# Performance work log

Measured on AMD Instinct MI355X. Metric: run time of the kernel, lower is better.

## Reference

```python
import jax, jax.numpy as jnp
import numpy as np

NUM_HOPS = 8
SIGMA = 0.1
EPS = 1e-12  # torch F.normalize default eps


def _l2_normalize(x):
    # torch.nn.functional.normalize(x, dim=1): x / max(||x||_2, eps)
    norm = jnp.linalg.norm(x, axis=1, keepdims=True)
    return x / jnp.maximum(norm, EPS)


def setup_inputs() -> dict:
    key = jax.random.key(0)
    k1, k2 = jax.random.split(key)
    N, E, D = 100000, 3200000, 128
    x = jax.random.normal(k1, (N, D), dtype=jnp.float32)
    edge_index = jax.random.randint(k2, (2, E), 0, N, dtype=jnp.int64)
    return {"x": x, "edge_index": edge_index}


def reference(x, edge_index):
    # A[i, j] = 1 for each edge (i=src, j=dst); A^T @ h scatters h[src] into rows dst.
    # Duplicate edges coalesce by summation, matching torch sparse mm.
    N = x.shape[0]
    src = edge_index[0]
    dst = edge_index[1]
    noise_key = jax.random.key(42)
    cur = _l2_normalize(x)
    outs = [cur]
    for k in range(NUM_HOPS):
        aggr = jax.ops.segment_sum(cur[src], dst, num_segments=N)  # [N, D]
        noise = SIGMA * jax.random.normal(jax.random.fold_in(noise_key, k), aggr.shape, dtype=aggr.dtype)
        cur = _l2_normalize(aggr + noise)
        outs.append(cur)
    return jnp.stack(outs)  # [num_hops+1, N, D]
```

## Files before the change

### kernel.cpp

```cpp
#include <hip/hip_runtime.h>
#include <hip/hip_bf16.h>
#include <hip/hip_fp16.h>
#include <stdint.h>

#define D 128
#define NUM_HOPS 8
#define SCAN_BS 256
#define SCAN2_BS 512
#define FILLA_EPT 16

__host__ __device__ inline void tf2x32(uint32_t k0, uint32_t k1,
                                       uint32_t x0, uint32_t x1,
                                       uint32_t* o0, uint32_t* o1) {
  uint32_t ks2 = k0 ^ k1 ^ 0x1BD11BDAu;
  x0 += k0; x1 += k1;
#define TF_RND(r) { x0 += x1; x1 = (x1 << r) | (x1 >> (32 - r)); x1 ^= x0; }
  TF_RND(13) TF_RND(15) TF_RND(26) TF_RND(6)
  x0 += k1; x1 += ks2 + 1u;
  TF_RND(17) TF_RND(29) TF_RND(16) TF_RND(24)
  x0 += ks2; x1 += k0 + 2u;
  TF_RND(13) TF_RND(15) TF_RND(26) TF_RND(6)
  x0 += k0; x1 += k1 + 3u;
  TF_RND(17) TF_RND(29) TF_RND(16) TF_RND(24)
  x0 += k1; x1 += ks2 + 4u;
  TF_RND(13) TF_RND(15) TF_RND(26) TF_RND(6)
  x0 += ks2; x1 += k0 + 5u;
#undef TF_RND
  *o0 = x0; *o1 = x1;
}

__device__ inline float erfinv_f32(float x) {
  float w = -log1pf(-x * x);
  float p;
  if (w < 5.0f) {
    w = w - 2.5f;
    p = 2.81022636e-08f;
    p = fmaf(p, w, 3.43273939e-07f);
    p = fmaf(p, w, -3.5233877e-06f);
    p = fmaf(p, w, -4.39150654e-06f);
    p = fmaf(p, w, 0.00021858087f);
    p = fmaf(p, w, -0.00125372503f);
    p = fmaf(p, w, -0.00417768164f);
    p = fmaf(p, w, 0.246640727f);
    p = fmaf(p, w, 1.50140941f);
  } else {
    w = sqrtf(w) - 3.0f;
    p = -0.000200214257f;
    p = fmaf(p, w, 0.000100950558f);
    p = fmaf(p, w, 0.00134934322f);
    p = fmaf(p, w, -0.00367342844f);
    p = fmaf(p, w, 0.00573950773f);
    p = fmaf(p, w, -0.0076224613f);
    p = fmaf(p, w, 0.00943887047f);
    p = fmaf(p, w, 1.00167406f);
    p = fmaf(p, w, 2.83297682f);
  }
  return p * x;
}

__device__ inline float noise_from_bits(uint32_t bits) {
  const float lo = -0.99999994f;
  uint32_t fb = (bits >> 9) | 0x3f800000u;
  float f = __uint_as_float(fb) - 1.0f;
  float u = fmaxf(lo, fmaf(f, 2.0f, lo));
  return 0.1f * (1.41421354f * erfinv_f32(u));
}

__device__ inline float noise_elem(uint32_t fk0, uint32_t fk1, long t) {
  uint32_t o0, o1;
  tf2x32(fk0, fk1, (uint32_t)(((unsigned long)t) >> 32), (uint32_t)t, &o0, &o1);
  return noise_from_bits(o0 ^ o1);
}

__device__ inline bool edges_are_i64(const int* __restrict__ ei) {
  return (ei[1] | ei[3] | ei[5] | ei[7] | ei[9] | ei[11] | ei[13] | ei[15]) == 0;
}

__global__ __launch_bounds__(256) void hist_kernel(const int* __restrict__ ei,
                                                   int* __restrict__ counts, long E) {
  long e = (long)blockIdx.x * blockDim.x + threadIdx.x;
  if (e >= E) return;
  bool i64 = edges_are_i64(ei);
  int d = __builtin_nontemporal_load(&ei[i64 ? (2 * (E + e)) : (E + e)]);
  atomicAdd(&counts[d], 1);
}

__global__ __launch_bounds__(SCAN_BS) void scan1_kernel(const int* __restrict__ counts,
                                                        int* __restrict__ excl,
                                                        int* __restrict__ partials, int N) {
  __shared__ int lds[SCAN_BS];
  int tid = threadIdx.x;
  int i = blockIdx.x * SCAN_BS + tid;
  int v = (i < N) ? counts[i] : 0;
  lds[tid] = v;
  __syncthreads();
  for (int off = 1; off < SCAN_BS; off <<= 1) {
    int t = (tid >= off) ? lds[tid - off] : 0;
    __syncthreads();
    if (tid >= off) lds[tid] += t;
    __syncthreads();
  }
  int incl = lds[tid];
  if (i < N) excl[i] = incl - v;
  if (tid == SCAN_BS - 1) partials[blockIdx.x] = incl;
}

__global__ __launch_bounds__(SCAN2_BS) void scan2_kernel(int* __restrict__ partials, int nchunks) {
  __shared__ int lds[SCAN2_BS];
  int tid = threadIdx.x;
  int v = (tid < nchunks) ? partials[tid] : 0;
  lds[tid] = v;
  __syncthreads();
  for (int off = 1; off < SCAN2_BS; off <<= 1) {
    int t = (tid >= off) ? lds[tid - off] : 0;
    __syncthreads();
    if (tid >= off) lds[tid] += t;
    __syncthreads();
  }
  if (tid < nchunks) partials[tid] = lds[tid] - v;
}

__global__ __launch_bounds__(256) void scan3_kernel(int* __restrict__ row_ptr,
                                                    const int* __restrict__ partials,
                                                    int* __restrict__ cursor, int N, int E) {
  int i = blockIdx.x * blockDim.x + threadIdx.x;
  if (i > N) return;
  if (i == N) { row_ptr[N] = E; return; }
  int v = row_ptr[i] + partials[i >> 8];
  row_ptr[i] = v;
  cursor[i] = v;
}

__global__ __launch_bounds__(256) void bucket_init_kernel(const int* __restrict__ row_ptr,
                                                          int* __restrict__ bucketCursor,
                                                          int nb, int shift, int N) {
  int b = blockIdx.x * blockDim.x + threadIdx.x;
  if (b >= nb) return;
  long r = (long)b << shift;
  if (r > N) r = N;
  bucketCursor[b] = row_ptr[r];
}

__global__ __launch_bounds__(256) void fillA_kernel(const int* __restrict__ ei,
                                                    int* __restrict__ bucketCursor,
                                                    uint64_t* __restrict__ tmp,
                                                    long E, int shift, int nb) {
  __shared__ int ldsCount[256];
  __shared__ int ldsBase[256];
  __shared__ int ldsRank[256];
  int tid = threadIdx.x;
  long base = (long)blockIdx.x * (256 * FILLA_EPT);
  bool i64 = edges_are_i64(ei);

  int  sv[FILLA_EPT], dv[FILLA_EPT];
  ldsCount[tid] = 0; ldsRank[tid] = 0;
  __syncthreads();

  #pragma unroll
  for (int j = 0; j < FILLA_EPT; ++j) {
    long e = base + tid + (long)j * 256;
    if (e < E) {
      sv[j] = __builtin_nontemporal_load(&ei[i64 ? (2 * e) : e]);
      dv[j] = __builtin_nontemporal_load(&ei[i64 ? (2 * (E + e)) : (E + e)]);
      atomicAdd(&ldsCount[dv[j] >> shift], 1);
    } else { sv[j] = -1; dv[j] = -1; }
  }
  __syncthreads();
  if (tid < nb && ldsCount[tid] > 0)
    ldsBase[tid] = atomicAdd(&bucketCursor[tid], ldsCount[tid]);
  __syncthreads();
  #pragma unroll
  for (int j = 0; j < FILLA_EPT; ++j) {
    if (dv[j] >= 0) {
      int b = dv[j] >> shift;
      int r = atomicAdd(&ldsRank[b], 1);
      tmp[ldsBase[b] + r] = ((uint64_t)(uint32_t)dv[j] << 32) | (uint32_t)sv[j];
    }
  }
}

__global__ __launch_bounds__(256) void fillB_kernel(const uint64_t* __restrict__ tmp,
                                                    const int* __restrict__ row_ptr,
                                                    int* __restrict__ cursor,
                                                    int* __restrict__ col,
                                                    int shift, int N) {
  int b = blockIdx.x;
  long r0 = (long)b << shift;
  long r1 = r0 + ((long)1 << shift);
  if (r0 > N) r0 = N;
  if (r1 > N) r1 = N;
  int beg = row_ptr[r0], end = row_ptr[r1];
  for (int i = beg + threadIdx.x; i < end; i += 256) {
    uint64_t e = __builtin_nontemporal_load(&tmp[i]);
    int d = (int)(e >> 32);
    int s = (int)(uint32_t)e;
    int slot = atomicAdd(&cursor[d], 1);
    col[slot] = s;
  }
}

__global__ __launch_bounds__(256) void fill_kernel(const int* __restrict__ ei,
                                                   int* __restrict__ cursor,
                                                   int* __restrict__ col, long E) {
  long e = (long)blockIdx.x * blockDim.x + threadIdx.x;
  if (e >= E) return;
  bool i64 = edges_are_i64(ei);
  int s = __builtin_nontemporal_load(&ei[i64 ? (2 * e) : e]);
  int d = __builtin_nontemporal_load(&ei[i64 ? (2 * (E + e)) : (E + e)]);
  int slot = atomicAdd(&cursor[d], 1);
  col[slot] = s;
}

__global__ __launch_bounds__(256) void norm0_kernel(const float* __restrict__ in,
                                                    float* __restrict__ out,
                                                    __half* __restrict__ mir, int N) {
  long t = (long)blockIdx.x * blockDim.x + threadIdx.x;
  int row = (int)(t >> 6);
  int lane = (int)(t & 63);
  if (row >= N) return;
  float2 v = *(const float2*)(in + (size_t)row * D + lane * 2);
  float s = v.x * v.x + v.y * v.y;
  #pragma unroll
  for (int off = 32; off > 0; off >>= 1) s += __shfl_xor(s, off, 64);
  float inv = 1.0f / fmaxf(sqrtf(s), 1e-12f);
  float2 o; o.x = v.x * inv; o.y = v.y * inv;
  *(float2*)(out + (size_t)row * D + lane * 2) = o;
  __half2 h = __float22half2_rn(o);
  ((uint32_t*)mir)[(size_t)row * 64 + lane] = *(const uint32_t*)&h;
}

__global__ __launch_bounds__(256) void gather_hop_f16(const __half* __restrict__ mirIn,
                                                      float* __restrict__ nxt,
                                                      __half* __restrict__ mirOut,
                                                      const int* __restrict__ row_ptr,
                                                      const int* __restrict__ col,
                                                      int N, uint32_t fk0, uint32_t fk1) {
  long t = (long)blockIdx.x * blockDim.x + threadIdx.x;
  int row = (int)(t >> 6);
  if (row >= N) return;
  int lane = (int)(t & 63);
  int q = lane >> 4;
  int l16 = lane & 15;

  long t0 = (long)row * D + 2 * lane;
  float n0 = noise_elem(fk0, fk1, t0);
  float n1 = noise_elem(fk0, fk1, t0 + 1);

  float acc[8];
  #pragma unroll
  for (int j = 0; j < 8; ++j) acc[j] = 0.f;

  auto acc8 = [&](uint4 a) {
    const __half2* hp = (const __half2*)&a;
    #pragma unroll
    for (int j = 0; j < 4; ++j) {
      float2 f = __half22float2(hp[j]);
      acc[2 * j]     += f.x;
      acc[2 * j + 1] += f.y;
    }
  };

  const uint4* mir4 = (const uint4*)mirIn;
  int beg = row_ptr[row], end = row_ptr[row + 1];
  int i = beg + q;
  for (; i + 4 < end; i += 8) {
    int s0 = col[i];
    int s1 = col[i + 4];
    uint4 a = mir4[(size_t)s0 * 16 + l16];
    uint4 b = mir4[(size_t)s1 * 16 + l16];
    acc8(a); acc8(b);
  }
  for (; i < end; i += 4) {
    int s = col[i];
    acc8(mir4[(size_t)s * 16 + l16]);
  }

  #pragma unroll
  for (int j = 0; j < 8; ++j) {
    acc[j] += __shfl_xor(acc[j], 16, 64);
    acc[j] += __shfl_xor(acc[j], 32, 64);
  }

  #pragma unroll
  for (int j = 0; j < 8; ++j) {
    int src = (l16 << 2) | (j >> 1);
    acc[j] += __shfl((j & 1) ? n1 : n0, src, 64);
  }

  float ss = 0.f;
  #pragma unroll
  for (int j = 0; j < 8; ++j) ss += acc[j] * acc[j];
  ss += __shfl_xor(ss, 1, 64);
  ss += __shfl_xor(ss, 2, 64);
  ss += __shfl_xor(ss, 4, 64);
  ss += __shfl_xor(ss, 8, 64);
  float inv = 1.0f / fmaxf(sqrtf(ss), 1e-12f);
  #pragma unroll
  for (int j = 0; j < 8; ++j) acc[j] *= inv;

  if (q == 0) {
    float4* op = (float4*)(nxt + (size_t)row * D + l16 * 8);
    op[0] = make_float4(acc[0], acc[1], acc[2], acc[3]);
    op[1] = make_float4(acc[4], acc[5], acc[6], acc[7]);
  } else if (q == 1) {
    __half2 h0 = __float22half2_rn(make_float2(acc[0], acc[1]));
    __half2 h1 = __float22half2_rn(make_float2(acc[2], acc[3]));
    __half2 h2 = __float22half2_rn(make_float2(acc[4], acc[5]));
    __half2 h3 = __float22half2_rn(make_float2(acc[6], acc[7]));
    uint4 u;
    u.x = *(const uint32_t*)&h0; u.y = *(const uint32_t*)&h1;
    u.z = *(const uint32_t*)&h2; u.w = *(const uint32_t*)&h3;
    ((uint4*)mirOut)[(size_t)row * 16 + l16] = u;
  }
}

__global__ __launch_bounds__(256) void gather_hop(const float* __restrict__ cur,
                                                  float* __restrict__ nxt,
                                                  const int* __restrict__ row_ptr,
                                                  const int* __restrict__ col,
                                                  int N, uint32_t fk0, uint32_t fk1) {
  long t = (long)blockIdx.x * blockDim.x + threadIdx.x;
  int row = (int)(t >> 6);
  if (row >= N) return;
  int lane = (int)(t & 63);
  int half = lane >> 5;
  int l32 = lane & 31;

  float4 acc = make_float4(0.f, 0.f, 0.f, 0.f);
  int beg = row_ptr[row], end = row_ptr[row + 1];
  int i = beg + half;
  for (; i + 6 < end; i += 8) {
    int s0 = col[i], s1 = col[i + 2], s2 = col[i + 4], s3 = col[i + 6];
    float4 v0 = ((const float4*)(cur + (size_t)s0 * D))[l32];
    float4 v1 = ((const float4*)(cur + (size_t)s1 * D))[l32];
    float4 v2 = ((const float4*)(cur + (size_t)s2 * D))[l32];
    float4 v3 = ((const float4*)(cur + (size_t)s3 * D))[l32];
    acc.x += v0.x + v1.x + v2.x + v3.x;
    acc.y += v0.y + v1.y + v2.y + v3.y;
    acc.z += v0.z + v1.z + v2.z + v3.z;
    acc.w += v0.w + v1.w + v2.w + v3.w;
  }
  for (; i < end; i += 2) {
    int s = col[i];
    float4 v = ((const float4*)(cur + (size_t)s * D))[l32];
    acc.x += v.x; acc.y += v.y; acc.z += v.z; acc.w += v.w;
  }
  acc.x += __shfl_xor(acc.x, 32, 64);
  acc.y += __shfl_xor(acc.y, 32, 64);
  acc.z += __shfl_xor(acc.z, 32, 64);
  acc.w += __shfl_xor(acc.w, 32, 64);

  long t0 = (long)row * D + l32 * 4;
  acc.x += noise_elem(fk0, fk1, t0);
  acc.y += noise_elem(fk0, fk1, t0 + 1);
  acc.z += noise_elem(fk0, fk1, t0 + 2);
  acc.w += noise_elem(fk0, fk1, t0 + 3);

  float ss = acc.x * acc.x + acc.y * acc.y + acc.z * acc.z + acc.w * acc.w;
  #pragma unroll
  for (int off = 16; off > 0; off >>= 1) ss += __shfl_xor(ss, off, 64);
  float inv = 1.0f / fmaxf(sqrtf(ss), 1e-12f);
  if (half == 0) {
    float4 o;
    o.x = acc.x * inv; o.y = acc.y * inv; o.z = acc.z * inv; o.w = acc.w * inv;
    ((float4*)(nxt + (size_t)row * D))[l32] = o;
  }
}

__global__ __launch_bounds__(256) void noise_kernel(float* __restrict__ out,
                                                    uint32_t fk0, uint32_t fk1, long n) {
  long t = (long)blockIdx.x * blockDim.x + threadIdx.x;
  if (t >= n) return;
  out[t] = noise_elem(fk0, fk1, t);
}

__global__ __launch_bounds__(256) void scatter_kernel(const float* __restrict__ cur,
                                                      float* __restrict__ aggr,
                                                      const int* __restrict__ ei, long E) {
  long tid = (long)blockIdx.x * blockDim.x + threadIdx.x;
  long e = tid >> 5;
  if (e >= E) return;
  int lane = (int)(tid & 31);
  bool i64 = edges_are_i64(ei);
  int s = ei[i64 ? (2 * e) : e];
  int d = ei[i64 ? (2 * (E + e)) : (E + e)];
  float4 v = *(const float4*)(cur + (size_t)s * D + lane * 4);
  float* dp = aggr + (size_t)d * D + lane * 4;
  unsafeAtomicAdd(dp + 0, v.x);
  unsafeAtomicAdd(dp + 1, v.y);
  unsafeAtomicAdd(dp + 2, v.z);
  unsafeAtomicAdd(dp + 3, v.w);
}

__global__ __launch_bounds__(256) void norm_kernel(const float* __restrict__ in,
                                                   float* __restrict__ out, int N) {
  long t = (long)blockIdx.x * blockDim.x + threadIdx.x;
  int row = (int)(t >> 6);
  int lane = (int)(t & 63);
  if (row >= N) return;
  float2 v = *(const float2*)(in + (size_t)row * D + lane * 2);
  float s = v.x * v.x + v.y * v.y;
  #pragma unroll
  for (int off = 32; off > 0; off >>= 1) s += __shfl_xor(s, off, 64);
  float inv = 1.0f / fmaxf(sqrtf(s), 1e-12f);
  float2 o; o.x = v.x * inv; o.y = v.y * inv;
  *(float2*)(out + (size_t)row * D + lane * 2) = o;
}

static inline size_t align_up(size_t v, size_t a) { return (v + a - 1) & ~(a - 1); }

extern "C" void kernel_launch(void* const* d_in, const int* in_sizes, int n_in,
                              void* d_out, int out_size, void* d_ws, size_t ws_size,
                              hipStream_t stream) {
  const float* x = (const float*)d_in[0];
  const int* ei = (const int*)d_in[1];
  const long N = in_sizes[0] / D;
  const long E = in_sizes[1] / 2;
  float* out = (float*)d_out;
  const long ND = N * D;

  uint32_t fk0[NUM_HOPS], fk1[NUM_HOPS];
  for (int k = 0; k < NUM_HOPS; ++k)
    tf2x32(0u, 42u, 0u, (uint32_t)k, &fk0[k], &fk1[k]);

  int shift = 9;
  while ((((N + ((long)1 << shift) - 1) >> shift)) > 256) shift++;
  const int nb = (int)((N + ((long)1 << shift) - 1) >> shift);
  const int nchunks = (int)((N + SCAN_BS - 1) / SCAN_BS);

  uintptr_t base = (uintptr_t)d_ws;
  size_t off = 0;
  auto carve = [&](size_t bytes, size_t align) -> uintptr_t {
    off = align_up(off, align);
    uintptr_t p = base + off;
    off += bytes;
    return p;
  };
  int* row_ptr      = (int*)carve((size_t)(N + 1) * 4, 256);
  int* counts       = (int*)carve((size_t)N * 4, 256);
  int* partials     = (int*)carve((size_t)nchunks * 4, 256);
  int* bucketCursor = (int*)carve((size_t)nb * 4, 256);
  int* col          = (int*)carve((size_t)E * 4, 256);
  size_t need_csr = off;
  uint64_t* tmp     = (uint64_t*)carve((size_t)E * 8, 256);
  size_t need_tmp = off;
  __half* mirA      = (__half*)carve((size_t)ND * 2, 256);
  __half* mirB      = (__half*)carve((size_t)ND * 2, 256);
  size_t need_full = off;

  long nthreads = N * 64;
  int ngrid = (int)((nthreads + 255) / 256);

  if (ws_size >= need_csr && nchunks <= SCAN2_BS) {
    (void)hipMemsetAsync(counts, 0, (size_t)N * sizeof(int), stream);
    hist_kernel<<<(int)((E + 255) / 256), 256, 0, stream>>>(ei, counts, E);
    scan1_kernel<<<nchunks, SCAN_BS, 0, stream>>>(counts, row_ptr, partials, (int)N);
    scan2_kernel<<<1, SCAN2_BS, 0, stream>>>(partials, nchunks);
    scan3_kernel<<<(int)((N + 256) / 256), 256, 0, stream>>>(row_ptr, partials, counts, (int)N, (int)E);

    bool have_tmp = (ws_size >= need_tmp);
    if (have_tmp) {
      bucket_init_kernel<<<(nb + 255) / 256, 256, 0, stream>>>(row_ptr, bucketCursor, nb, shift, (int)N);
      long epw = 256L * FILLA_EPT;
      fillA_kernel<<<(int)((E + epw - 1) / epw), 256, 0, stream>>>(ei, bucketCursor, tmp, E, shift, nb);
      fillB_kernel<<<nb, 256, 0, stream>>>(tmp, row_ptr, counts, col, shift, (int)N);
    } else {
      fill_kernel<<<(int)((E + 255) / 256), 256, 0, stream>>>(ei, counts, col, E);
    }

    if (ws_size >= need_full) {
      norm0_kernel<<<ngrid, 256, 0, stream>>>(x, out, mirA, (int)N);
      for (int k = 0; k < NUM_HOPS; ++k) {
        float* nxt = out + (size_t)(k + 1) * ND;
        const __half* mi = (k & 1) ? mirB : mirA;
        __half* mo       = (k & 1) ? mirA : mirB;
        gather_hop_f16<<<ngrid, 256, 0, stream>>>(mi, nxt, mo, row_ptr, col,
                                                  (int)N, fk0[k], fk1[k]);
      }
    } else if (!have_tmp && ws_size >= need_csr + 2 * (size_t)ND * sizeof(__half) + 512) {
      __half* mA = (__half*)((char*)align_up((size_t)((char*)d_ws - (char*)0) + need_csr, 256));
      mA = (__half*)((char*)d_ws + (align_up(need_csr, 256) - 0));
      __half* mB = mA + ND;
      norm0_kernel<<<ngrid, 256, 0, stream>>>(x, out, mA, (int)N);
      for (int k = 0; k < NUM_HOPS; ++k) {
        float* nxt = out + (size_t)(k + 1) * ND;
        const __half* mi = (k & 1) ? mB : mA;
        __half* mo       = (k & 1) ? mA : mB;
        gather_hop_f16<<<ngrid, 256, 0, stream>>>(mi, nxt, mo, row_ptr, col,
                                                  (int)N, fk0[k], fk1[k]);
      }
    } else {
      norm_kernel<<<ngrid, 256, 0, stream>>>(x, out, (int)N);
      for (int k = 0; k < NUM_HOPS; ++k) {
        const float* cur = out + (size_t)k * ND;
        float* nxt = out + (size_t)(k + 1) * ND;
        gather_hop<<<ngrid, 256, 0, stream>>>(cur, nxt, row_ptr, col, (int)N, fk0[k], fk1[k]);
      }
    }
  } else {
    norm_kernel<<<ngrid, 256, 0, stream>>>(x, out, (int)N);
    for (int k = 0; k < NUM_HOPS; ++k) {
      const float* cur = out + (size_t)k * ND;
      float* nxt = out + (size_t)(k + 1) * ND;
      noise_kernel<<<(int)((ND + 255) / 256), 256, 0, stream>>>(nxt, fk0[k], fk1[k], ND);
      long sthreads = E * 32;
      scatter_kernel<<<(int)((sthreads + 255) / 256), 256, 0, stream>>>(cur, nxt, ei, E);
      norm_kernel<<<ngrid, 256, 0, stream>>>(nxt, nxt, (int)N);
    }
  }
}
```

Baseline: 1.198 ms.

## Build CSR via bucket histogram and per-bucket LDS counting, drop global histogram

```diff
diff --git a/kernel.cpp b/kernel.cpp
--- a/kernel.cpp
+++ b/kernel.cpp
@@ -1,13 +1,14 @@
 #include <hip/hip_runtime.h>
-#include <hip/hip_bf16.h>
 #include <hip/hip_fp16.h>
 #include <stdint.h>
 
 #define D 128
 #define NUM_HOPS 8
-#define SCAN_BS 256
-#define SCAN2_BS 512
 #define FILLA_EPT 16
+
+typedef float f32x2 __attribute__((ext_vector_type(2)));
+typedef float f32x4 __attribute__((ext_vector_type(4)));
+typedef unsigned int u32x4 __attribute__((ext_vector_type(4)));
 
 __host__ __device__ inline void tf2x32(uint32_t k0, uint32_t k1,
                                        uint32_t x0, uint32_t x1,
@@ -76,69 +77,49 @@
   return (ei[1] | ei[3] | ei[5] | ei[7] | ei[9] | ei[11] | ei[13] | ei[15]) == 0;
 }
 
-__global__ __launch_bounds__(256) void hist_kernel(const int* __restrict__ ei,
-                                                   int* __restrict__ counts, long E) {
-  long e = (long)blockIdx.x * blockDim.x + threadIdx.x;
-  if (e >= E) return;
+__global__ __launch_bounds__(256) void zero256_kernel(int* __restrict__ p) {
+  p[threadIdx.x] = 0;
+}
+
+__global__ __launch_bounds__(256) void bucket_hist_kernel(const int* __restrict__ ei,
+                                                          int* __restrict__ bucketCount,
+                                                          long E, int shift) {
+  __shared__ int cnt[256];
+  int tid = threadIdx.x;
+  cnt[tid] = 0;
+  __syncthreads();
+  long base = (long)blockIdx.x * (256 * FILLA_EPT);
   bool i64 = edges_are_i64(ei);
-  int d = __builtin_nontemporal_load(&ei[i64 ? (2 * (E + e)) : (E + e)]);
-  atomicAdd(&counts[d], 1);
-}
-
-__global__ __launch_bounds__(SCAN_BS) void scan1_kernel(const int* __restrict__ counts,
-                                                        int* __restrict__ excl,
-                                                        int* __restrict__ partials, int N) {
-  __shared__ int lds[SCAN_BS];
+  #pragma unroll
+  for (int j = 0; j < FILLA_EPT; ++j) {
+    long e = base + tid + (long)j * 256;
+    if (e < E) {
+      int d = __builtin_nontemporal_load(&ei[i64 ? (2 * (E + e)) : (E + e)]);
+      atomicAdd(&cnt[d >> shift], 1);
+    }
+  }
+  __syncthreads();
+  if (cnt[tid] > 0) atomicAdd(&bucketCount[tid], cnt[tid]);
+}
+
+__global__ __launch_bounds__(256) void bucket_scan_kernel(const int* __restrict__ bucketCount,
+                                                          int* __restrict__ bucketBase,
+                                                          int* __restrict__ bucketCursor,
+                                                          int nb, int E) {
+  __shared__ int lds[256];
   int tid = threadIdx.x;
-  int i = blockIdx.x * SCAN_BS + tid;
-  int v = (i < N) ? counts[i] : 0;
+  int v = (tid < nb) ? bucketCount[tid] : 0;
   lds[tid] = v;
   __syncthreads();
-  for (int off = 1; off < SCAN_BS; off <<= 1) {
+  for (int off = 1; off < 256; off <<= 1) {
     int t = (tid >= off) ? lds[tid - off] : 0;
     __syncthreads();
-    if (tid >= off) lds[tid] += t;
+    lds[tid] += t;
     __syncthreads();
   }
-  int incl = lds[tid];
-  if (i < N) excl[i] = incl - v;
-  if (tid == SCAN_BS - 1) partials[blockIdx.x] = incl;
-}
-
-__global__ __launch_bounds__(SCAN2_BS) void scan2_kernel(int* __restrict__ partials, int nchunks) {
-  __shared__ int lds[SCAN2_BS];
-  int tid = threadIdx.x;
-  int v = (tid < nchunks) ? partials[tid] : 0;
-  lds[tid] = v;
-  __syncthreads();
-  for (int off = 1; off < SCAN2_BS; off <<= 1) {
-    int t = (tid >= off) ? lds[tid - off] : 0;
-    __syncthreads();
-    if (tid >= off) lds[tid] += t;
-    __syncthreads();
-  }
-  if (tid < nchunks) partials[tid] = lds[tid] - v;
-}
-
-__global__ __launch_bounds__(256) void scan3_kernel(int* __restrict__ row_ptr,
-                                                    const int* __restrict__ partials,
-                                                    int* __restrict__ cursor, int N, int E) {
-  int i = blockIdx.x * blockDim.x + threadIdx.x;
-  if (i > N) return;
-  if (i == N) { row_ptr[N] = E; return; }
-  int v = row_ptr[i] + partials[i >> 8];
-  row_ptr[i] = v;
-  cursor[i] = v;
-}
-
-__global__ __launch_bounds__(256) void bucket_init_kernel(const int* __restrict__ row_ptr,
-                                                          int* __restrict__ bucketCursor,
-                                                          int nb, int shift, int N) {
-  int b = blockIdx.x * blockDim.x + threadIdx.x;
-  if (b >= nb) return;
-  long r = (long)b << shift;
-  if (r > N) r = N;
-  bucketCursor[b] = row_ptr[r];
+  int excl = lds[tid] - v;
+  if (tid < nb) { bucketBase[tid] = excl; bucketCursor[tid] = excl; }
+  if (tid == 0) bucketBase[nb] = E;
 }
 
 __global__ __launch_bounds__(256) void fillA_kernel(const int* __restrict__ ei,
@@ -152,7 +133,7 @@
   long base = (long)blockIdx.x * (256 * FILLA_EPT);
   bool i64 = edges_are_i64(ei);
 
-  int  sv[FILLA_EPT], dv[FILLA_EPT];
+  int sv[FILLA_EPT], dv[FILLA_EPT];
   ldsCount[tid] = 0; ldsRank[tid] = 0;
   __syncthreads();
 
@@ -179,36 +160,54 @@
   }
 }
 
-__global__ __launch_bounds__(256) void fillB_kernel(const uint64_t* __restrict__ tmp,
-                                                    const int* __restrict__ row_ptr,
-                                                    int* __restrict__ cursor,
-                                                    int* __restrict__ col,
-                                                    int shift, int N) {
+__global__ __launch_bounds__(256) void fillB2_kernel(const uint64_t* __restrict__ tmp,
+                                                     const int* __restrict__ bucketBase,
+                                                     int* __restrict__ row_ptr,
+                                                     int* __restrict__ col,
+                                                     int shift, int N, int nb) {
+  __shared__ int h[512];
+  __shared__ int ex[512];
+  __shared__ int ps[256];
   int b = blockIdx.x;
-  long r0 = (long)b << shift;
-  long r1 = r0 + ((long)1 << shift);
-  if (r0 > N) r0 = N;
-  if (r1 > N) r1 = N;
-  int beg = row_ptr[r0], end = row_ptr[r1];
-  for (int i = beg + threadIdx.x; i < end; i += 256) {
+  int tid = threadIdx.x;
+  int r0 = b << shift;
+  int bs = 1 << shift;
+  int rows = N - r0; if (rows > bs) rows = bs;
+  int beg = bucketBase[b], end = bucketBase[b + 1];
+
+  h[tid] = 0; h[tid + 256] = 0;
+  __syncthreads();
+  for (int i = beg + tid; i < end; i += 256) {
     uint64_t e = __builtin_nontemporal_load(&tmp[i]);
-    int d = (int)(e >> 32);
-    int s = (int)(uint32_t)e;
-    int slot = atomicAdd(&cursor[d], 1);
-    col[slot] = s;
-  }
-}
-
-__global__ __launch_bounds__(256) void fill_kernel(const int* __restrict__ ei,
-                                                   int* __restrict__ cursor,
-                                                   int* __restrict__ col, long E) {
-  long e = (long)blockIdx.x * blockDim.x + threadIdx.x;
-  if (e >= E) return;
-  bool i64 = edges_are_i64(ei);
-  int s = __builtin_nontemporal_load(&ei[i64 ? (2 * e) : e]);
-  int d = __builtin_nontemporal_load(&ei[i64 ? (2 * (E + e)) : (E + e)]);
-  int slot = atomicAdd(&cursor[d], 1);
-  col[slot] = s;
+    int r = (int)(e >> 32) - r0;
+    atomicAdd(&h[r], 1);
+  }
+  __syncthreads();
+  int a = h[2 * tid], c = h[2 * tid + 1];
+  ps[tid] = a + c;
+  __syncthreads();
+  for (int off = 1; off < 256; off <<= 1) {
+    int t = (tid >= off) ? ps[tid - off] : 0;
+    __syncthreads();
+    ps[tid] += t;
+    __syncthreads();
+  }
+  int pe = ps[tid] - (a + c);
+  ex[2 * tid] = pe;
+  ex[2 * tid + 1] = pe + a;
+  __syncthreads();
+  for (int r = tid; r < bs; r += 256) {
+    if (r < rows) row_ptr[r0 + r] = beg + ex[r];
+    h[r] = ex[r];
+  }
+  if (b == nb - 1 && tid == 0) row_ptr[N] = end;
+  __syncthreads();
+  for (int i = beg + tid; i < end; i += 256) {
+    uint64_t e = __builtin_nontemporal_load(&tmp[i]);
+    int r = (int)(e >> 32) - r0;
+    int slot = beg + atomicAdd(&h[r], 1);
+    col[slot] = (int)(uint32_t)e;
+  }
 }
 
 __global__ __launch_bounds__(256) void norm0_kernel(const float* __restrict__ in,
@@ -223,9 +222,9 @@
   #pragma unroll
   for (int off = 32; off > 0; off >>= 1) s += __shfl_xor(s, off, 64);
   float inv = 1.0f / fmaxf(sqrtf(s), 1e-12f);
-  float2 o; o.x = v.x * inv; o.y = v.y * inv;
-  *(float2*)(out + (size_t)row * D + lane * 2) = o;
-  __half2 h = __float22half2_rn(o);
+  f32x2 o; o.x = v.x * inv; o.y = v.y * inv;
+  __builtin_nontemporal_store(o, (f32x2*)(out + (size_t)row * D + lane * 2));
+  __half2 h = __float22half2_rn(make_float2(o.x, o.y));
   ((uint32_t*)mir)[(size_t)row * 64 + lane] = *(const uint32_t*)&h;
 }
 
@@ -264,14 +263,14 @@
   int beg = row_ptr[row], end = row_ptr[row + 1];
   int i = beg + q;
   for (; i + 4 < end; i += 8) {
-    int s0 = col[i];
-    int s1 = col[i + 4];
+    int s0 = __builtin_nontemporal_load(&col[i]);
+    int s1 = __builtin_nontemporal_load(&col[i + 4]);
     uint4 a = mir4[(size_t)s0 * 16 + l16];
     uint4 b = mir4[(size_t)s1 * 16 + l16];
     acc8(a); acc8(b);
   }
   for (; i < end; i += 4) {
-    int s = col[i];
+    int s = __builtin_nontemporal_load(&col[i]);
     acc8(mir4[(size_t)s * 16 + l16]);
   }
 
@@ -299,71 +298,19 @@
   for (int j = 0; j < 8; ++j) acc[j] *= inv;
 
   if (q == 0) {
-    float4* op = (float4*)(nxt + (size_t)row * D + l16 * 8);
-    op[0] = make_float4(acc[0], acc[1], acc[2], acc[3]);
-    op[1] = make_float4(acc[4], acc[5], acc[6], acc[7]);
+    f32x4 o0 = {acc[0], acc[1], acc[2], acc[3]};
+    f32x4 o1 = {acc[4], acc[5], acc[6], acc[7]};
+    f32x4* op = (f32x4*)(nxt + (size_t)row * D + l16 * 8);
+    __builtin_nontemporal_store(o0, op);
+    __builtin_nontemporal_store(o1, op + 1);
   } else if (q == 1) {
     __half2 h0 = __float22half2_rn(make_float2(acc[0], acc[1]));
     __half2 h1 = __float22half2_rn(make_float2(acc[2], acc[3]));
     __half2 h2 = __float22half2_rn(make_float2(acc[4], acc[5]));
     __half2 h3 = __float22half2_rn(make_float2(acc[6], acc[7]));
-    uint4 u;
-    u.x = *(const uint32_t*)&h0; u.y = *(const uint32_t*)&h1;
-    u.z = *(const uint32_t*)&h2; u.w = *(const uint32_t*)&h3;
-    ((uint4*)mirOut)[(size_t)row * 16 + l16] = u;
-  }
-}
-
-__global__ __launch_bounds__(256) void gather_hop(const float* __restrict__ cur,
-                                                  float* __restrict__ nxt,
-                                                  const int* __restrict__ row_ptr,
-                                                  const int* __restrict__ col,
-                                                  int N, uint32_t fk0, uint32_t fk1) {
-  long t = (long)blockIdx.x * blockDim.x + threadIdx.x;
-  int row = (int)(t >> 6);
-  if (row >= N) return;
-  int lane = (int)(t & 63);
-  int half = lane >> 5;
-  int l32 = lane & 31;
-
-  float4 acc = make_float4(0.f, 0.f, 0.f, 0.f);
-  int beg = row_ptr[row], end = row_ptr[row + 1];
-  int i = beg + half;
-  for (; i + 6 < end; i += 8) {
-    int s0 = col[i], s1 = col[i + 2], s2 = col[i + 4], s3 = col[i + 6];
-    float4 v0 = ((const float4*)(cur + (size_t)s0 * D))[l32];
-    float4 v1 = ((const float4*)(cur + (size_t)s1 * D))[l32];
-    float4 v2 = ((const float4*)(cur + (size_t)s2 * D))[l32];
-    float4 v3 = ((const float4*)(cur + (size_t)s3 * D))[l32];
-    acc.x += v0.x + v1.x + v2.x + v3.x;
-    acc.y += v0.y + v1.y + v2.y + v3.y;
-    acc.z += v0.z + v1.z + v2.z + v3.z;
-    acc.w += v0.w + v1.w + v2.w + v3.w;
-  }
-  for (; i < end; i += 2) {
-    int s = col[i];
-    float4 v = ((const float4*)(cur + (size_t)s * D))[l32];
-    acc.x += v.x; acc.y += v.y; acc.z += v.z; acc.w += v.w;
-  }
-  acc.x += __shfl_xor(acc.x, 32, 64);
-  acc.y += __shfl_xor(acc.y, 32, 64);
-  acc.z += __shfl_xor(acc.z, 32, 64);
-  acc.w += __shfl_xor(acc.w, 32, 64);
-
-  long t0 = (long)row * D + l32 * 4;
-  acc.x += noise_elem(fk0, fk1, t0);
-  acc.y += noise_elem(fk0, fk1, t0 + 1);
-  acc.z += noise_elem(fk0, fk1, t0 + 2);
-  acc.w += noise_elem(fk0, fk1, t0 + 3);
-
-  float ss = acc.x * acc.x + acc.y * acc.y + acc.z * acc.z + acc.w * acc.w;
-  #pragma unroll
-  for (int off = 16; off > 0; off >>= 1) ss += __shfl_xor(ss, off, 64);
-  float inv = 1.0f / fmaxf(sqrtf(ss), 1e-12f);
-  if (half == 0) {
-    float4 o;
-    o.x = acc.x * inv; o.y = acc.y * inv; o.z = acc.z * inv; o.w = acc.w * inv;
-    ((float4*)(nxt + (size_t)row * D))[l32] = o;
+    u32x4 u = { *(const uint32_t*)&h0, *(const uint32_t*)&h1,
+                *(const uint32_t*)&h2, *(const uint32_t*)&h3 };
+    __builtin_nontemporal_store(u, (u32x4*)mirOut + ((size_t)row * 16 + l16));
   }
 }
 
@@ -426,7 +373,7 @@
   int shift = 9;
   while ((((N + ((long)1 << shift) - 1) >> shift)) > 256) shift++;
   const int nb = (int)((N + ((long)1 << shift) - 1) >> shift);
-  const int nchunks = (int)((N + SCAN_BS - 1) / SCAN_BS);
+  const int bs = 1 << shift;
 
   uintptr_t base = (uintptr_t)d_ws;
   size_t off = 0;
@@ -437,13 +384,11 @@
     return p;
   };
   int* row_ptr      = (int*)carve((size_t)(N + 1) * 4, 256);
-  int* counts       = (int*)carve((size_t)N * 4, 256);
-  int* partials     = (int*)carve((size_t)nchunks * 4, 256);
+  int* bucketCount  = (int*)carve(256 * 4, 256);
+  int* bucketBase   = (int*)carve((size_t)(nb + 1) * 4, 256);
   int* bucketCursor = (int*)carve((size_t)nb * 4, 256);
   int* col          = (int*)carve((size_t)E * 4, 256);
-  size_t need_csr = off;
   uint64_t* tmp     = (uint64_t*)carve((size_t)E * 8, 256);
-  size_t need_tmp = off;
   __half* mirA      = (__half*)carve((size_t)ND * 2, 256);
   __half* mirB      = (__half*)carve((size_t)ND * 2, 256);
   size_t need_full = off;
@@ -451,51 +396,22 @@
   long nthreads = N * 64;
   int ngrid = (int)((nthreads + 255) / 256);
 
-  if (ws_size >= need_csr && nchunks <= SCAN2_BS) {
-    (void)hipMemsetAsync(counts, 0, (size_t)N * sizeof(int), stream);
-    hist_kernel<<<(int)((E + 255) / 256), 256, 0, stream>>>(ei, counts, E);
-    scan1_kernel<<<nchunks, SCAN_BS, 0, stream>>>(counts, row_ptr, partials, (int)N);
-    scan2_kernel<<<1, SCAN2_BS, 0, stream>>>(partials, nchunks);
-    scan3_kernel<<<(int)((N + 256) / 256), 256, 0, stream>>>(row_ptr, partials, counts, (int)N, (int)E);
-
-    bool have_tmp = (ws_size >= need_tmp);
-    if (have_tmp) {
-      bucket_init_kernel<<<(nb + 255) / 256, 256, 0, stream>>>(row_ptr, bucketCursor, nb, shift, (int)N);
-      long epw = 256L * FILLA_EPT;
-      fillA_kernel<<<(int)((E + epw - 1) / epw), 256, 0, stream>>>(ei, bucketCursor, tmp, E, shift, nb);
-      fillB_kernel<<<nb, 256, 0, stream>>>(tmp, row_ptr, counts, col, shift, (int)N);
-    } else {
-      fill_kernel<<<(int)((E + 255) / 256), 256, 0, stream>>>(ei, counts, col, E);
-    }
-
-    if (ws_size >= need_full) {
-      norm0_kernel<<<ngrid, 256, 0, stream>>>(x, out, mirA, (int)N);
-      for (int k = 0; k < NUM_HOPS; ++k) {
-        float* nxt = out + (size_t)(k + 1) * ND;
-        const __half* mi = (k & 1) ? mirB : mirA;
-        __half* mo       = (k & 1) ? mirA : mirB;
-        gather_hop_f16<<<ngrid, 256, 0, stream>>>(mi, nxt, mo, row_ptr, col,
-                                                  (int)N, fk0[k], fk1[k]);
-      }
-    } else if (!have_tmp && ws_size >= need_csr + 2 * (size_t)ND * sizeof(__half) + 512) {
-      __half* mA = (__half*)((char*)align_up((size_t)((char*)d_ws - (char*)0) + need_csr, 256));
-      mA = (__half*)((char*)d_ws + (align_up(need_csr, 256) - 0));
-      __half* mB = mA + ND;
-      norm0_kernel<<<ngrid, 256, 0, stream>>>(x, out, mA, (int)N);
-      for (int k = 0; k < NUM_HOPS; ++k) {
-        float* nxt = out + (size_t)(k + 1) * ND;
-        const __half* mi = (k & 1) ? mB : mA;
-        __half* mo       = (k & 1) ? mA : mB;
-        gather_hop_f16<<<ngrid, 256, 0, stream>>>(mi, nxt, mo, row_ptr, col,
-                                                  (int)N, fk0[k], fk1[k]);
-      }
-    } else {
-      norm_kernel<<<ngrid, 256, 0, stream>>>(x, out, (int)N);
-      for (int k = 0; k < NUM_HOPS; ++k) {
-        const float* cur = out + (size_t)k * ND;
-        float* nxt = out + (size_t)(k + 1) * ND;
-        gather_hop<<<ngrid, 256, 0, stream>>>(cur, nxt, row_ptr, col, (int)N, fk0[k], fk1[k]);
-      }
+  if (ws_size >= need_full && nb <= 256 && bs <= 512) {
+    long epw = 256L * FILLA_EPT;
+    int nblk = (int)((E + epw - 1) / epw);
+    zero256_kernel<<<1, 256, 0, stream>>>(bucketCount);
+    bucket_hist_kernel<<<nblk, 256, 0, stream>>>(ei, bucketCount, E, shift);
+    bucket_scan_kernel<<<1, 256, 0, stream>>>(bucketCount, bucketBase, bucketCursor, nb, (int)E);
+    fillA_kernel<<<nblk, 256, 0, stream>>>(ei, bucketCursor, tmp, E, shift, nb);
+    fillB2_kernel<<<nb, 256, 0, stream>>>(tmp, bucketBase, row_ptr, col, shift, (int)N, nb);
+
+    norm0_kernel<<<ngrid, 256, 0, stream>>>(x, out, mirA, (int)N);
+    for (int k = 0; k < NUM_HOPS; ++k) {
+      float* nxt = out + (size_t)(k + 1) * ND;
+      const __half* mi = (k & 1) ? mirB : mirA;
+      __half* mo       = (k & 1) ? mirA : mirB;
+      gather_hop_f16<<<ngrid, 256, 0, stream>>>(mi, nxt, mo, row_ptr, col,
+                                                (int)N, fk0[k], fk1[k]);
     }
   } else {
     norm_kernel<<<ngrid, 256, 0, stream>>>(x, out, (int)N);
```

New measurement: 1.139 ms (median of 2 runs). 1.05x faster.
